# Optimization experiments

Measured on AMD Instinct MI355X. Metric: run time of the kernel, lower is better.

The kernel has to match this reference:

```python
import jax, jax.numpy as jnp
import numpy as np

B, H, W, C = 8, 32, 32, 256
HEADS, UNITS = 8, 256
OUT_D = UNITS // HEADS          # 32
HID_D = int(OUT_D * 1.0)        # 32 (hidden_rate=1.0)


def setup_inputs() -> dict:
    key = jax.random.key(0)
    ks = jax.random.split(key, 8)
    glorot_qk = np.sqrt(6.0 / (C + HID_D)).astype(np.float32)
    glorot_v = np.sqrt(6.0 / (C + OUT_D)).astype(np.float32)
    return {
        "seq": jax.random.normal(ks[0], (B, H, W, C), dtype=jnp.float32),
        "ctx": jax.random.normal(ks[1], (B, H, W, C), dtype=jnp.float32),
        "Wq": jax.random.uniform(ks[2], (HEADS, C, HID_D), jnp.float32, -glorot_qk, glorot_qk),
        "Wk": jax.random.uniform(ks[3], (HEADS, C, HID_D), jnp.float32, -glorot_qk, glorot_qk),
        "Wv": jax.random.uniform(ks[4], (HEADS, C, OUT_D), jnp.float32, -glorot_v, glorot_v),
        "bq": jnp.zeros((HEADS, HID_D), jnp.float32),
        "bk": jnp.zeros((HEADS, HID_D), jnp.float32),
        "bv": jnp.zeros((HEADS, OUT_D), jnp.float32),
    }


def reference(seq, ctx, Wq, Wk, Wv, bq, bk, bv):
    # NB: the original layer computes q, k, v all from `seq`; `ctx` only fixes
    # the weight shapes. Dropout omitted (inference / deterministic baseline).
    b, h, w, c = seq.shape
    n = h * w
    s = seq.reshape(b, n, c)
    q = jnp.einsum("bnc,hcd->bhnd", s, Wq) + bq[None, :, None, :]
    k = jnp.einsum("bnc,hcd->bhnd", s, Wk) + bk[None, :, None, :]
    v = jnp.einsum("bnc,hcd->bhnd", s, Wv) + bv[None, :, None, :]
    scale = 1.0 / jnp.sqrt(jnp.asarray(k.shape[-1], k.dtype))
    logits = jnp.einsum("bhnd,bhmd->bhnm", q, k * scale)  # [B,heads,N,N]
    attn = jax.nn.softmax(logits, axis=-1)
    a = jnp.einsum("bhnm,bhmd->bhnd", attn, jnp.tanh(v))  # tanh on V, as in source
    out = a.transpose(0, 2, 1, 3).reshape(b, h, w, -1)     # concat heads on channel
    return out
```

## Files before the change

### kernel.cpp

```cpp
#include <hip/hip_runtime.h>
#include <hip/hip_bf16.h>

typedef __attribute__((ext_vector_type(8))) short bf16x8_t;
typedef __attribute__((ext_vector_type(4))) float f32x4_t;
typedef __attribute__((ext_vector_type(16))) float f32x16_t;
typedef __attribute__((ext_vector_type(4))) unsigned short u16x4_t;
typedef __attribute__((ext_vector_type(2))) unsigned u32x2_t;

#define DEVINL __device__ __forceinline__

static constexpr int CN   = 256;
static constexpr int NSEQ = 1024;
static constexpr int NH   = 8;
static constexpr float QSCALE = 0.17677669529663687f * 1.4426950408889634f;

DEVINL unsigned short f2bf(float f) {
    union { __hip_bfloat16 h; unsigned short u; } cv;
    cv.h = __float2bfloat16(f);
    return cv.u;
}

DEVINL unsigned cvtpk_bf16(float lo, float hi) {
    unsigned r;
    asm("v_cvt_pk_bf16_f32 %0, %1, %2" : "=v"(r) : "v"(lo), "v"(hi));
    return r;
}

DEVINL float partner32_f(float x, int h2) {
    unsigned u = __builtin_bit_cast(unsigned, x);
    u32x2_t r = __builtin_amdgcn_permlane32_swap(u, u, false, false);
    return __builtin_bit_cast(float, h2 ? r.x : r.y);
}

DEVINL float fast_tanh(float x) {
    x = fminf(fmaxf(x, -20.f), 20.f);
    float t = __builtin_amdgcn_exp2f(2.8853900817779268f * x);
    return (t - 1.f) * __builtin_amdgcn_rcpf(t + 1.f);
}

__global__ void prep_kernel(const float* __restrict__ Wq, const float* __restrict__ Wk,
                            const float* __restrict__ Wv, const float* __restrict__ seq,
                            unsigned short* __restrict__ Wbt, unsigned short* __restrict__ Sb) {
    if (blockIdx.x < 768) {
        int idx  = blockIdx.x * 256 + threadIdx.x;
        int c    = idx & 255;
        int ncol = idx >> 8;
        int h = ncol / 96, r = ncol % 96;
        int t = r >> 5, d = r & 31;
        const float* W = (t == 0) ? Wq : (t == 1) ? Wk : Wv;
        Wbt[idx] = f2bf(W[((h << 8) + c) * 32 + d]);
    } else {
        int i = (blockIdx.x - 768) * 256 + threadIdx.x;
        const float4 x = ((const float4*)seq)[2 * i];
        const float4 y = ((const float4*)seq)[2 * i + 1];
        bf16x8_t r;
        r[0] = (short)f2bf(x.x); r[1] = (short)f2bf(x.y);
        r[2] = (short)f2bf(x.z); r[3] = (short)f2bf(x.w);
        r[4] = (short)f2bf(y.x); r[5] = (short)f2bf(y.y);
        r[6] = (short)f2bf(y.z); r[7] = (short)f2bf(y.w);
        *(bf16x8_t*)(Sb + (size_t)i * 8) = r;
    }
}

__global__ __launch_bounds__(256) void proj_kernel(
        const unsigned short* __restrict__ Sb, const unsigned short* __restrict__ Wbt,
        const float* __restrict__ bq, const float* __restrict__ bk, const float* __restrict__ bv,
        unsigned short* __restrict__ Qs, unsigned short* __restrict__ Kf,
        unsigned short* __restrict__ Vf) {
    const int w    = threadIdx.x >> 6;
    const int lane = threadIdx.x & 63;
    const int l15  = lane & 15, l4 = lane >> 4;
    const int mw = blockIdx.y * 64 + (w >> 1) * 32;
    const int nw = blockIdx.x * 128 + (w & 1) * 64;

    f32x4_t acc[2][4];
    for (int mg = 0; mg < 2; ++mg)
        for (int g = 0; g < 4; ++g)
            acc[mg][g] = (f32x4_t){0.f, 0.f, 0.f, 0.f};

#pragma unroll
    for (int k0 = 0; k0 < CN; k0 += 32) {
        const int kk = k0 + l4 * 8;
        bf16x8_t a[2], b[4];
        for (int mg = 0; mg < 2; ++mg)
            a[mg] = *(const bf16x8_t*)(Sb + (size_t)(mw + mg * 16 + l15) * CN + kk);
        for (int g = 0; g < 4; ++g)
            b[g] = *(const bf16x8_t*)(Wbt + (size_t)(nw + g * 16 + l15) * CN + kk);
        for (int mg = 0; mg < 2; ++mg)
            for (int g = 0; g < 4; ++g)
                acc[mg][g] = __builtin_amdgcn_mfma_f32_16x16x32_bf16(a[mg], b[g], acc[mg][g], 0, 0, 0);
    }

    for (int g = 0; g < 4; ++g) {
        const int ncol = nw + g * 16;
        const int h = ncol / 96, r = ncol % 96;
        const int t = r >> 5;
        const int d = (r & 31) + l15;
        for (int mg = 0; mg < 2; ++mg) {
            const int m0 = mw + mg * 16 + l4 * 4;
            const int b_ = m0 >> 10;
            const int n0 = m0 & 1023;
            const int bh = b_ * NH + h;
            const int kt = n0 >> 5;
            if (t == 2) {
                const float bias = bv[h * 32 + d];
                u16x4_t vs;
                for (int i = 0; i < 4; ++i)
                    vs[i] = f2bf(fast_tanh(acc[mg][g][i] + bias));
                const size_t fidx = ((size_t)(bh * 32 + kt) * 2 + ((n0 >> 4) & 1)) * 64
                                    + d + 32 * ((n0 >> 3) & 1);
                *(u16x4_t*)(Vf + fidx * 8 + (n0 & 7)) = vs;
            } else if (t == 0) {
                const float bias = bq[h * 32 + d];
                for (int i = 0; i < 4; ++i)
                    Qs[((size_t)bh * NSEQ + n0 + i) * 32 + d] = f2bf((acc[mg][g][i] + bias) * QSCALE);
            } else {
                const float bias = bk[h * 32 + d];
                const size_t fbase = (((size_t)(bh * 32 + kt) * 2 + (d >> 4)) * 64
                                      + 32 * ((d >> 3) & 1)) * 8 + (d & 7);
                for (int i = 0; i < 4; ++i)
                    Kf[fbase + (size_t)((n0 + i) & 31) * 8] = f2bf(acc[mg][g][i] + bias);
            }
        }
    }
}

__global__ __launch_bounds__(256, 4) void attn_kernel(
        const unsigned short* __restrict__ Qs, const unsigned short* __restrict__ Kf,
        const unsigned short* __restrict__ Vf, float* __restrict__ out) {
    __shared__ float comb[2][64][17];
    const int lane = threadIdx.x & 63;
    const int w    = threadIdx.x >> 6;
    const int l31  = lane & 31;
    const int h2   = lane >> 5;
    const int qsel = w >> 1, ksel = w & 1;
    const int bh   = blockIdx.x;
    const int b_   = bh >> 3, h = bh & 7;
    const int qrow = blockIdx.y * 64 + qsel * 32 + l31;

    const unsigned short* Qp = Qs + ((size_t)bh * NSEQ + qrow) * 32 + h2 * 8;
    const bf16x8_t qf0 = *(const bf16x8_t*)(Qp);
    const bf16x8_t qf1 = *(const bf16x8_t*)(Qp + 16);

    const unsigned short* Kp = Kf + (size_t)bh * 32768 + ksel * 16384 + lane * 8;
    const unsigned short* Vp = Vf + (size_t)bh * 32768 + ksel * 16384 + lane * 8;

    f32x16_t o = {0.f,0.f,0.f,0.f,0.f,0.f,0.f,0.f,0.f,0.f,0.f,0.f,0.f,0.f,0.f,0.f};
    float l_acc = 0.f;

    bf16x8_t kf0 = *(const bf16x8_t*)(Kp);
    bf16x8_t kf1 = *(const bf16x8_t*)(Kp + 512);
    bf16x8_t va0 = *(const bf16x8_t*)(Vp);
    bf16x8_t va1 = *(const bf16x8_t*)(Vp + 512);

#pragma unroll
    for (int kt = 0; kt < 16; ++kt) {
        const int ktn = (kt + 1) & 15;
        bf16x8_t nk0 = *(const bf16x8_t*)(Kp + ktn * 1024);
        bf16x8_t nk1 = *(const bf16x8_t*)(Kp + ktn * 1024 + 512);
        bf16x8_t nv0 = *(const bf16x8_t*)(Vp + ktn * 1024);
        bf16x8_t nv1 = *(const bf16x8_t*)(Vp + ktn * 1024 + 512);

        f32x16_t st = {0.f,0.f,0.f,0.f,0.f,0.f,0.f,0.f,0.f,0.f,0.f,0.f,0.f,0.f,0.f,0.f};
        __builtin_amdgcn_s_setprio(1);
        st = __builtin_amdgcn_mfma_f32_32x32x16_bf16(kf0, qf0, st, 0, 0, 0);
        st = __builtin_amdgcn_mfma_f32_32x32x16_bf16(kf1, qf1, st, 0, 0, 0);
        __builtin_amdgcn_s_setprio(0);

        float p[16];
#pragma unroll
        for (int r = 0; r < 16; ++r) p[r] = __builtin_amdgcn_exp2f(st[r]);

        float s8[8];
#pragma unroll
        for (int g = 0; g < 8; ++g) s8[g] = p[2 * g] + p[2 * g + 1];
        float s4a = s8[0] + s8[1], s4b = s8[2] + s8[3];
        float s4c = s8[4] + s8[5], s4d = s8[6] + s8[7];
        l_acc += (s4a + s4b) + (s4c + s4d);

        unsigned pw[8];
#pragma unroll
        for (int g = 0; g < 8; ++g)
            pw[g] = cvtpk_bf16(p[2 * g], p[2 * g + 1]);

        u32x2_t s02 = __builtin_amdgcn_permlane32_swap(pw[0], pw[2], false, false);
        u32x2_t s13 = __builtin_amdgcn_permlane32_swap(pw[1], pw[3], false, false);
        u32x2_t s46 = __builtin_amdgcn_permlane32_swap(pw[4], pw[6], false, false);
        u32x2_t s57 = __builtin_amdgcn_permlane32_swap(pw[5], pw[7], false, false);
        union { unsigned u[4]; bf16x8_t v; } pb1, pb2;
        pb1.u[0] = s02.x; pb1.u[1] = s13.x; pb1.u[2] = s02.y; pb1.u[3] = s13.y;
        pb2.u[0] = s46.x; pb2.u[1] = s57.x; pb2.u[2] = s46.y; pb2.u[3] = s57.y;

        __builtin_amdgcn_s_setprio(1);
        o = __builtin_amdgcn_mfma_f32_32x32x16_bf16(va0, pb1.v, o, 0, 0, 0);
        o = __builtin_amdgcn_mfma_f32_32x32x16_bf16(va1, pb2.v, o, 0, 0, 0);
        __builtin_amdgcn_s_setprio(0);

        kf0 = nk0; kf1 = nk1; va0 = nv0; va1 = nv1;
    }

    const float l_half = l_acc + partner32_f(l_acc, h2);

    if (ksel) {
#pragma unroll
        for (int r = 0; r < 16; ++r) comb[qsel][lane][r] = o[r];
        comb[qsel][lane][16] = l_half;
    }
    __syncthreads();
    if (!ksel) {
        const float* c = comb[qsel][lane];
        const float inv = 1.0f / (l_half + c[16]);
        float* op = out + ((size_t)(b_ * NSEQ + qrow)) * 256 + h * 32 + h2 * 4;
#pragma unroll
        for (int g = 0; g < 4; ++g) {
            float4 q4;
            q4.x = (o[4 * g + 0] + c[4 * g + 0]) * inv;
            q4.y = (o[4 * g + 1] + c[4 * g + 1]) * inv;
            q4.z = (o[4 * g + 2] + c[4 * g + 2]) * inv;
            q4.w = (o[4 * g + 3] + c[4 * g + 3]) * inv;
            *(float4*)(op + 8 * g) = q4;
        }
    }
}

extern "C" void kernel_launch(void* const* d_in, const int* in_sizes, int n_in,
                              void* d_out, int out_size, void* d_ws, size_t ws_size,
                              hipStream_t stream) {
    const float* seq = (const float*)d_in[0];
    const float* Wq = (const float*)d_in[2];
    const float* Wk = (const float*)d_in[3];
    const float* Wv = (const float*)d_in[4];
    const float* bq = (const float*)d_in[5];
    const float* bk = (const float*)d_in[6];
    const float* bv = (const float*)d_in[7];
    float* out = (float*)d_out;

    char* ws = (char*)d_ws;
    unsigned short* Wbt = (unsigned short*)ws;
    unsigned short* Qs  = (unsigned short*)(ws + 393216);
    unsigned short* Kf  = (unsigned short*)(ws + 393216 + 4194304);
    unsigned short* Vf  = (unsigned short*)(ws + 393216 + 2 * 4194304);
    unsigned short* Sb  = (unsigned short*)(ws + 393216 + 3 * 4194304);

    hipLaunchKernelGGL(prep_kernel, dim3(1792), dim3(256), 0, stream, Wq, Wk, Wv, seq, Wbt, Sb);
    hipLaunchKernelGGL(proj_kernel, dim3(6, 128), dim3(256), 0, stream,
                       Sb, Wbt, bq, bk, bv, Qs, Kf, Vf);
    hipLaunchKernelGGL(attn_kernel, dim3(64, 16), dim3(256), 0, stream, Qs, Kf, Vf, out);
}
```

Measured before the change: 46.41 us.

## Fuse seq bf16 conversion into projection and triple-buffer K/V loads

```diff
diff --git a/kernel.cpp b/kernel.cpp
--- a/kernel.cpp
+++ b/kernel.cpp
@@ -39,31 +39,18 @@
 }
 
 __global__ void prep_kernel(const float* __restrict__ Wq, const float* __restrict__ Wk,
-                            const float* __restrict__ Wv, const float* __restrict__ seq,
-                            unsigned short* __restrict__ Wbt, unsigned short* __restrict__ Sb) {
-    if (blockIdx.x < 768) {
-        int idx  = blockIdx.x * 256 + threadIdx.x;
-        int c    = idx & 255;
-        int ncol = idx >> 8;
-        int h = ncol / 96, r = ncol % 96;
-        int t = r >> 5, d = r & 31;
-        const float* W = (t == 0) ? Wq : (t == 1) ? Wk : Wv;
-        Wbt[idx] = f2bf(W[((h << 8) + c) * 32 + d]);
-    } else {
-        int i = (blockIdx.x - 768) * 256 + threadIdx.x;
-        const float4 x = ((const float4*)seq)[2 * i];
-        const float4 y = ((const float4*)seq)[2 * i + 1];
-        bf16x8_t r;
-        r[0] = (short)f2bf(x.x); r[1] = (short)f2bf(x.y);
-        r[2] = (short)f2bf(x.z); r[3] = (short)f2bf(x.w);
-        r[4] = (short)f2bf(y.x); r[5] = (short)f2bf(y.y);
-        r[6] = (short)f2bf(y.z); r[7] = (short)f2bf(y.w);
-        *(bf16x8_t*)(Sb + (size_t)i * 8) = r;
-    }
+                            const float* __restrict__ Wv, unsigned short* __restrict__ Wbt) {
+    int idx  = blockIdx.x * 256 + threadIdx.x;
+    int c    = idx & 255;
+    int ncol = idx >> 8;
+    int h = ncol / 96, r = ncol % 96;
+    int t = r >> 5, d = r & 31;
+    const float* W = (t == 0) ? Wq : (t == 1) ? Wk : Wv;
+    Wbt[idx] = f2bf(W[((h << 8) + c) * 32 + d]);
 }
 
 __global__ __launch_bounds__(256) void proj_kernel(
-        const unsigned short* __restrict__ Sb, const unsigned short* __restrict__ Wbt,
+        const float* __restrict__ seq, const unsigned short* __restrict__ Wbt,
         const float* __restrict__ bq, const float* __restrict__ bk, const float* __restrict__ bv,
         unsigned short* __restrict__ Qs, unsigned short* __restrict__ Kf,
         unsigned short* __restrict__ Vf) {
@@ -82,8 +69,17 @@
     for (int k0 = 0; k0 < CN; k0 += 32) {
         const int kk = k0 + l4 * 8;
         bf16x8_t a[2], b[4];
-        for (int mg = 0; mg < 2; ++mg)
-            a[mg] = *(const bf16x8_t*)(Sb + (size_t)(mw + mg * 16 + l15) * CN + kk);
+        for (int mg = 0; mg < 2; ++mg) {
+            const float* p = seq + (size_t)(mw + mg * 16 + l15) * CN + kk;
+            const float4 x = *(const float4*)p;
+            const float4 y = *(const float4*)(p + 4);
+            union { unsigned u[4]; bf16x8_t v; } av;
+            av.u[0] = cvtpk_bf16(x.x, x.y);
+            av.u[1] = cvtpk_bf16(x.z, x.w);
+            av.u[2] = cvtpk_bf16(y.x, y.y);
+            av.u[3] = cvtpk_bf16(y.z, y.w);
+            a[mg] = av.v;
+        }
         for (int g = 0; g < 4; ++g)
             b[g] = *(const bf16x8_t*)(Wbt + (size_t)(nw + g * 16 + l15) * CN + kk);
         for (int mg = 0; mg < 2; ++mg)
@@ -148,23 +144,30 @@
     f32x16_t o = {0.f,0.f,0.f,0.f,0.f,0.f,0.f,0.f,0.f,0.f,0.f,0.f,0.f,0.f,0.f,0.f};
     float l_acc = 0.f;
 
-    bf16x8_t kf0 = *(const bf16x8_t*)(Kp);
-    bf16x8_t kf1 = *(const bf16x8_t*)(Kp + 512);
-    bf16x8_t va0 = *(const bf16x8_t*)(Vp);
-    bf16x8_t va1 = *(const bf16x8_t*)(Vp + 512);
+    bf16x8_t kbuf[3][2], vbuf[3][2];
+#pragma unroll
+    for (int t = 0; t < 2; ++t) {
+        kbuf[t][0] = *(const bf16x8_t*)(Kp + t * 1024);
+        kbuf[t][1] = *(const bf16x8_t*)(Kp + t * 1024 + 512);
+        vbuf[t][0] = *(const bf16x8_t*)(Vp + t * 1024);
+        vbuf[t][1] = *(const bf16x8_t*)(Vp + t * 1024 + 512);
+    }
 
 #pragma unroll
     for (int kt = 0; kt < 16; ++kt) {
-        const int ktn = (kt + 1) & 15;
-        bf16x8_t nk0 = *(const bf16x8_t*)(Kp + ktn * 1024);
-        bf16x8_t nk1 = *(const bf16x8_t*)(Kp + ktn * 1024 + 512);
-        bf16x8_t nv0 = *(const bf16x8_t*)(Vp + ktn * 1024);
-        bf16x8_t nv1 = *(const bf16x8_t*)(Vp + ktn * 1024 + 512);
+        const int cs = kt % 3;
+        const int ns = (kt + 2) % 3;
+        if (kt < 14) {
+            kbuf[ns][0] = *(const bf16x8_t*)(Kp + (kt + 2) * 1024);
+            kbuf[ns][1] = *(const bf16x8_t*)(Kp + (kt + 2) * 1024 + 512);
+            vbuf[ns][0] = *(const bf16x8_t*)(Vp + (kt + 2) * 1024);
+            vbuf[ns][1] = *(const bf16x8_t*)(Vp + (kt + 2) * 1024 + 512);
+        }
 
         f32x16_t st = {0.f,0.f,0.f,0.f,0.f,0.f,0.f,0.f,0.f,0.f,0.f,0.f,0.f,0.f,0.f,0.f};
         __builtin_amdgcn_s_setprio(1);
-        st = __builtin_amdgcn_mfma_f32_32x32x16_bf16(kf0, qf0, st, 0, 0, 0);
-        st = __builtin_amdgcn_mfma_f32_32x32x16_bf16(kf1, qf1, st, 0, 0, 0);
+        st = __builtin_amdgcn_mfma_f32_32x32x16_bf16(kbuf[cs][0], qf0, st, 0, 0, 0);
+        st = __builtin_amdgcn_mfma_f32_32x32x16_bf16(kbuf[cs][1], qf1, st, 0, 0, 0);
         __builtin_amdgcn_s_setprio(0);
 
         float p[16];
@@ -192,11 +195,9 @@
         pb2.u[0] = s46.x; pb2.u[1] = s57.x; pb2.u[2] = s46.y; pb2.u[3] = s57.y;
 
         __builtin_amdgcn_s_setprio(1);
-        o = __builtin_amdgcn_mfma_f32_32x32x16_bf16(va0, pb1.v, o, 0, 0, 0);
-        o = __builtin_amdgcn_mfma_f32_32x32x16_bf16(va1, pb2.v, o, 0, 0, 0);
+        o = __builtin_amdgcn_mfma_f32_32x32x16_bf16(vbuf[cs][0], pb1.v, o, 0, 0, 0);
+        o = __builtin_amdgcn_mfma_f32_32x32x16_bf16(vbuf[cs][1], pb2.v, o, 0, 0, 0);
         __builtin_amdgcn_s_setprio(0);
-
-        kf0 = nk0; kf1 = nk1; va0 = nv0; va1 = nv1;
     }
 
     const float l_half = l_acc + partner32_f(l_acc, h2);
@@ -240,10 +241,9 @@
     unsigned short* Qs  = (unsigned short*)(ws + 393216);
     unsigned short* Kf  = (unsigned short*)(ws + 393216 + 4194304);
     unsigned short* Vf  = (unsigned short*)(ws + 393216 + 2 * 4194304);
-    unsigned short* Sb  = (unsigned short*)(ws + 393216 + 3 * 4194304);
-
-    hipLaunchKernelGGL(prep_kernel, dim3(1792), dim3(256), 0, stream, Wq, Wk, Wv, seq, Wbt, Sb);
+
+    hipLaunchKernelGGL(prep_kernel, dim3(768), dim3(256), 0, stream, Wq, Wk, Wv, Wbt);
     hipLaunchKernelGGL(proj_kernel, dim3(6, 128), dim3(256), 0, stream,
-                       Sb, Wbt, bq, bk, bv, Qs, Kf, Vf);
+                       seq, Wbt, bq, bk, bv, Qs, Kf, Vf);
     hipLaunchKernelGGL(attn_kernel, dim3(64, 16), dim3(256), 0, stream, Qs, Kf, Vf, out);
 }
```

Measured after the change: 51.67 us. 1.11x slower.

## Share K/V tiles between query waves via double-buffered LDS exchange

Applied to the files above, without the earlier changes.

```diff
diff --git a/kernel.cpp b/kernel.cpp
--- a/kernel.cpp
+++ b/kernel.cpp
@@ -53,12 +53,12 @@
         int i = (blockIdx.x - 768) * 256 + threadIdx.x;
         const float4 x = ((const float4*)seq)[2 * i];
         const float4 y = ((const float4*)seq)[2 * i + 1];
-        bf16x8_t r;
-        r[0] = (short)f2bf(x.x); r[1] = (short)f2bf(x.y);
-        r[2] = (short)f2bf(x.z); r[3] = (short)f2bf(x.w);
-        r[4] = (short)f2bf(y.x); r[5] = (short)f2bf(y.y);
-        r[6] = (short)f2bf(y.z); r[7] = (short)f2bf(y.w);
-        *(bf16x8_t*)(Sb + (size_t)i * 8) = r;
+        union { unsigned u[4]; bf16x8_t v8; } rv;
+        rv.u[0] = cvtpk_bf16(x.x, x.y);
+        rv.u[1] = cvtpk_bf16(x.z, x.w);
+        rv.u[2] = cvtpk_bf16(y.x, y.y);
+        rv.u[3] = cvtpk_bf16(y.z, y.w);
+        *(bf16x8_t*)(Sb + (size_t)i * 8) = rv.v8;
     }
 }
 
@@ -125,10 +125,82 @@
     }
 }
 
+template<int QSEL>
+DEVINL void attn_half(const unsigned short* __restrict__ ownp,
+                      unsigned short* lds_own, const unsigned short* lds_oth,
+                      const int lane, const bf16x8_t qf0, const bf16x8_t qf1,
+                      f32x16_t& o, float& l_acc) {
+    bf16x8_t own0 = *(const bf16x8_t*)(ownp);
+    bf16x8_t own1 = *(const bf16x8_t*)(ownp + 512);
+    *(bf16x8_t*)(lds_own + lane * 8)       = own0;
+    *(bf16x8_t*)(lds_own + 512 + lane * 8) = own1;
+    __syncthreads();
+
+#pragma unroll
+    for (int kt = 0; kt < 16; ++kt) {
+        const int cur = kt & 1;
+        bf16x8_t n0, n1;
+        if (kt < 15) {
+            n0 = *(const bf16x8_t*)(ownp + (kt + 1) * 1024);
+            n1 = *(const bf16x8_t*)(ownp + (kt + 1) * 1024 + 512);
+        }
+        const bf16x8_t oth0 = *(const bf16x8_t*)(lds_oth + cur * 1024 + lane * 8);
+        const bf16x8_t oth1 = *(const bf16x8_t*)(lds_oth + cur * 1024 + 512 + lane * 8);
+
+        const bf16x8_t kf0 = QSEL ? oth0 : own0;
+        const bf16x8_t kf1 = QSEL ? oth1 : own1;
+        const bf16x8_t va0 = QSEL ? own0 : oth0;
+        const bf16x8_t va1 = QSEL ? own1 : oth1;
+
+        f32x16_t st = {0.f,0.f,0.f,0.f,0.f,0.f,0.f,0.f,0.f,0.f,0.f,0.f,0.f,0.f,0.f,0.f};
+        __builtin_amdgcn_s_setprio(1);
+        st = __builtin_amdgcn_mfma_f32_32x32x16_bf16(kf0, qf0, st, 0, 0, 0);
+        st = __builtin_amdgcn_mfma_f32_32x32x16_bf16(kf1, qf1, st, 0, 0, 0);
+        __builtin_amdgcn_s_setprio(0);
+
+        float p[16];
+#pragma unroll
+        for (int r = 0; r < 16; ++r) p[r] = __builtin_amdgcn_exp2f(st[r]);
+
+        float s8[8];
+#pragma unroll
+        for (int g = 0; g < 8; ++g) s8[g] = p[2 * g] + p[2 * g + 1];
+        float s4a = s8[0] + s8[1], s4b = s8[2] + s8[3];
+        float s4c = s8[4] + s8[5], s4d = s8[6] + s8[7];
+        l_acc += (s4a + s4b) + (s4c + s4d);
+
+        unsigned pw[8];
+#pragma unroll
+        for (int g = 0; g < 8; ++g)
+            pw[g] = cvtpk_bf16(p[2 * g], p[2 * g + 1]);
+
+        u32x2_t s02 = __builtin_amdgcn_permlane32_swap(pw[0], pw[2], false, false);
+        u32x2_t s13 = __builtin_amdgcn_permlane32_swap(pw[1], pw[3], false, false);
+        u32x2_t s46 = __builtin_amdgcn_permlane32_swap(pw[4], pw[6], false, false);
+        u32x2_t s57 = __builtin_amdgcn_permlane32_swap(pw[5], pw[7], false, false);
+        union { unsigned u[4]; bf16x8_t v; } pb1, pb2;
+        pb1.u[0] = s02.x; pb1.u[1] = s13.x; pb1.u[2] = s02.y; pb1.u[3] = s13.y;
+        pb2.u[0] = s46.x; pb2.u[1] = s57.x; pb2.u[2] = s46.y; pb2.u[3] = s57.y;
+
+        __builtin_amdgcn_s_setprio(1);
+        o = __builtin_amdgcn_mfma_f32_32x32x16_bf16(va0, pb1.v, o, 0, 0, 0);
+        o = __builtin_amdgcn_mfma_f32_32x32x16_bf16(va1, pb2.v, o, 0, 0, 0);
+        __builtin_amdgcn_s_setprio(0);
+
+        if (kt < 15) {
+            *(bf16x8_t*)(lds_own + (cur ^ 1) * 1024 + lane * 8)       = n0;
+            *(bf16x8_t*)(lds_own + (cur ^ 1) * 1024 + 512 + lane * 8) = n1;
+            own0 = n0; own1 = n1;
+        }
+        __syncthreads();
+    }
+}
+
 __global__ __launch_bounds__(256, 4) void attn_kernel(
         const unsigned short* __restrict__ Qs, const unsigned short* __restrict__ Kf,
         const unsigned short* __restrict__ Vf, float* __restrict__ out) {
     __shared__ float comb[2][64][17];
+    __shared__ __attribute__((aligned(16))) unsigned short tiles[2][2][2][1024];
     const int lane = threadIdx.x & 63;
     const int w    = threadIdx.x >> 6;
     const int l31  = lane & 31;
@@ -142,62 +214,15 @@
     const bf16x8_t qf0 = *(const bf16x8_t*)(Qp);
     const bf16x8_t qf1 = *(const bf16x8_t*)(Qp + 16);
 
-    const unsigned short* Kp = Kf + (size_t)bh * 32768 + ksel * 16384 + lane * 8;
-    const unsigned short* Vp = Vf + (size_t)bh * 32768 + ksel * 16384 + lane * 8;
+    const unsigned short* ownp = (qsel ? Vf : Kf) + (size_t)bh * 32768 + ksel * 16384 + lane * 8;
+    unsigned short* lds_own       = &tiles[qsel][ksel][0][0];
+    const unsigned short* lds_oth = &tiles[qsel ^ 1][ksel][0][0];
 
     f32x16_t o = {0.f,0.f,0.f,0.f,0.f,0.f,0.f,0.f,0.f,0.f,0.f,0.f,0.f,0.f,0.f,0.f};
     float l_acc = 0.f;
 
-    bf16x8_t kf0 = *(const bf16x8_t*)(Kp);
-    bf16x8_t kf1 = *(const bf16x8_t*)(Kp + 512);
-    bf16x8_t va0 = *(const bf16x8_t*)(Vp);
-    bf16x8_t va1 = *(const bf16x8_t*)(Vp + 512);
-
-#pragma unroll
-    for (int kt = 0; kt < 16; ++kt) {
-        const int ktn = (kt + 1) & 15;
-        bf16x8_t nk0 = *(const bf16x8_t*)(Kp + ktn * 1024);
-        bf16x8_t nk1 = *(const bf16x8_t*)(Kp + ktn * 1024 + 512);
-        bf16x8_t nv0 = *(const bf16x8_t*)(Vp + ktn * 1024);
-        bf16x8_t nv1 = *(const bf16x8_t*)(Vp + ktn * 1024 + 512);
-
-        f32x16_t st = {0.f,0.f,0.f,0.f,0.f,0.f,0.f,0.f,0.f,0.f,0.f,0.f,0.f,0.f,0.f,0.f};
-        __builtin_amdgcn_s_setprio(1);
-        st = __builtin_amdgcn_mfma_f32_32x32x16_bf16(kf0, qf0, st, 0, 0, 0);
-        st = __builtin_amdgcn_mfma_f32_32x32x16_bf16(kf1, qf1, st, 0, 0, 0);
-        __builtin_amdgcn_s_setprio(0);
-
-        float p[16];
-#pragma unroll
-        for (int r = 0; r < 16; ++r) p[r] = __builtin_amdgcn_exp2f(st[r]);
-
-        float s8[8];
-#pragma unroll
-        for (int g = 0; g < 8; ++g) s8[g] = p[2 * g] + p[2 * g + 1];
-        float s4a = s8[0] + s8[1], s4b = s8[2] + s8[3];
-        float s4c = s8[4] + s8[5], s4d = s8[6] + s8[7];
-        l_acc += (s4a + s4b) + (s4c + s4d);
-
-        unsigned pw[8];
-#pragma unroll
-        for (int g = 0; g < 8; ++g)
-            pw[g] = cvtpk_bf16(p[2 * g], p[2 * g + 1]);
-
-        u32x2_t s02 = __builtin_amdgcn_permlane32_swap(pw[0], pw[2], false, false);
-        u32x2_t s13 = __builtin_amdgcn_permlane32_swap(pw[1], pw[3], false, false);
-        u32x2_t s46 = __builtin_amdgcn_permlane32_swap(pw[4], pw[6], false, false);
-        u32x2_t s57 = __builtin_amdgcn_permlane32_swap(pw[5], pw[7], false, false);
-        union { unsigned u[4]; bf16x8_t v; } pb1, pb2;
-        pb1.u[0] = s02.x; pb1.u[1] = s13.x; pb1.u[2] = s02.y; pb1.u[3] = s13.y;
-        pb2.u[0] = s46.x; pb2.u[1] = s57.x; pb2.u[2] = s46.y; pb2.u[3] = s57.y;
-
-        __builtin_amdgcn_s_setprio(1);
-        o = __builtin_amdgcn_mfma_f32_32x32x16_bf16(va0, pb1.v, o, 0, 0, 0);
-        o = __builtin_amdgcn_mfma_f32_32x32x16_bf16(va1, pb2.v, o, 0, 0, 0);
-        __builtin_amdgcn_s_setprio(0);
-
-        kf0 = nk0; kf1 = nk1; va0 = nv0; va1 = nv1;
-    }
+    if (qsel == 0) attn_half<0>(ownp, lds_own, lds_oth, lane, qf0, qf1, o, l_acc);
+    else           attn_half<1>(ownp, lds_own, lds_oth, lane, qf0, qf1, o, l_acc);
 
     const float l_half = l_acc + partner32_f(l_acc, h2);
 
```

After: 48.40 us. +4.3%, slower.
